# Performance work log

Measured on AMD Instinct MI355X. Metric: run time of the kernel, lower is better.

## Reference

```python
import jax, jax.numpy as jnp
import numpy as np

B, S, D, H = 2, 2048, 1024, 16
DH = D // H
DFF = 4 * D
EPS = 1e-5


def layer_norm(x, w, b):
    m = jnp.mean(x, axis=-1, keepdims=True)
    v = jnp.mean((x - m) ** 2, axis=-1, keepdims=True)
    return (x - m) / jnp.sqrt(v + EPS) * w + b


def setup_inputs() -> dict:
    key = jax.random.key(0)
    ks = jax.random.split(key, 12)
    s = 0.02
    x = jax.random.normal(ks[0], (B, S, D), dtype=jnp.float32)
    mask = jnp.tril(jnp.ones((S, S), dtype=jnp.int32))  # causal mask, 0 = blocked
    Wq = jax.random.normal(ks[1], (H, D, DH), dtype=jnp.float32) * s
    Wk = jax.random.normal(ks[2], (H, D, DH), dtype=jnp.float32) * s
    Wv = jax.random.normal(ks[3], (H, D, DH), dtype=jnp.float32) * s
    Wo = jax.random.normal(ks[4], (D, D), dtype=jnp.float32) * s
    bo = jnp.zeros((D,), dtype=jnp.float32)
    W1 = jax.random.normal(ks[5], (D, DFF), dtype=jnp.float32) * s
    b1 = jnp.zeros((DFF,), dtype=jnp.float32)
    W2 = jax.random.normal(ks[6], (DFF, D), dtype=jnp.float32) * s
    b2 = jnp.zeros((D,), dtype=jnp.float32)
    ln1_w = jnp.ones((D,), dtype=jnp.float32)
    ln1_b = jnp.zeros((D,), dtype=jnp.float32)
    ln2_w = jnp.ones((D,), dtype=jnp.float32)
    ln2_b = jnp.zeros((D,), dtype=jnp.float32)
    return {"x": x, "mask": mask, "Wq": Wq, "Wk": Wk, "Wv": Wv, "Wo": Wo,
            "bo": bo, "W1": W1, "b1": b1, "W2": W2, "b2": b2,
            "ln1_w": ln1_w, "ln1_b": ln1_b, "ln2_w": ln2_w, "ln2_b": ln2_b}


def reference(x, mask, Wq, Wk, Wv, Wo, bo, W1, b1, W2, b2,
              ln1_w, ln1_b, ln2_w, ln2_b):
    # --- pre-LN attention ---
    xn = layer_norm(x, ln1_w, ln1_b)
    q = jnp.einsum('bsd,hdk->bhsk', xn, Wq)  # [B,H,S,DH]
    k = jnp.einsum('bsd,hdk->bhsk', xn, Wk)
    v = jnp.einsum('bsd,hdk->bhsk', xn, Wv)
    scores = jnp.einsum('bhik,bhjk->bhij', q, k) / jnp.sqrt(jnp.float32(DH))
    scores = jnp.where(mask == 0, jnp.float32(-1e9), scores)  # mask broadcasts [S,S]->[B,H,S,S]
    attn = jax.nn.softmax(scores, axis=-1)
    o = jnp.einsum('bhij,bhjk->bhik', attn, v)        # [B,H,S,DH]
    o = o.transpose(0, 2, 1, 3).reshape(x.shape[0], x.shape[1], D)  # concat heads
    attn_out = o @ Wo + bo
    x = x + attn_out
    # --- pre-LN FFN ---
    xn2 = layer_norm(x, ln2_w, ln2_b)
    h = jax.nn.relu(xn2 @ W1 + b1)
    x = x + (h @ W2 + b2)
    return x
```

## Files before the change

### kernel.cpp

```cpp
#include <hip/hip_runtime.h>
#include <hip/hip_bf16.h>
#include <stdint.h>

#define DEV static __device__ __forceinline__

using f32x4  = __attribute__((ext_vector_type(4))) float;
using bf16x8 = __attribute__((ext_vector_type(8))) __bf16;

constexpr int SEQ = 2048;

DEV unsigned short f2bf(float f) {
  union { float f; unsigned u; } c; c.f = f;
  unsigned u = c.u;
  u += 0x7fffu + ((u >> 16) & 1u);
  return (unsigned short)(u >> 16);
}

DEV float wred_sum(float v) {
  #pragma unroll
  for (int m = 32; m > 0; m >>= 1) v += __shfl_xor(v, m, 64);
  return v;
}

DEV void g2l16(const unsigned short* g, unsigned short* l) {
  __builtin_amdgcn_global_load_lds(
      (const __attribute__((address_space(1))) void*)g,
      (__attribute__((address_space(3))) void*)l, 16, 0, 0);
}

DEV int xcd_map(int bid, int nwg) {
  const int cpx = nwg >> 3;
  return (bid & 7) * cpx + (bid >> 3);
}

__global__ __launch_bounds__(256) void convw_kernel(
    const float* __restrict__ in, unsigned short* __restrict__ out,
    int K, int Nh)
{
  const int h = blockIdx.z;
  const float* inh = in + (size_t)h * K * Nh;
  unsigned short* outh = out + (size_t)h * Nh * K;
  const int n0 = blockIdx.x * 32, k0 = blockIdx.y * 32;
  __shared__ float t[32][33];
  const int tx = threadIdx.x & 31, ty = threadIdx.x >> 5;
  #pragma unroll
  for (int r = 0; r < 32; r += 8)
    t[ty + r][tx] = inh[(size_t)(k0 + ty + r) * Nh + (n0 + tx)];
  __syncthreads();
  #pragma unroll
  for (int r = 0; r < 32; r += 8)
    outh[(size_t)(n0 + ty + r) * K + (k0 + tx)] = f2bf(t[tx][ty + r]);
}

__global__ __launch_bounds__(256) void ln_kernel(
    const float* __restrict__ x, const float* __restrict__ w,
    const float* __restrict__ b, unsigned short* __restrict__ out)
{
  const int row = blockIdx.x;
  const int tid = threadIdx.x;
  const float4 v = ((const float4*)(x + (size_t)row * 1024))[tid];
  float s  = v.x + v.y + v.z + v.w;
  float s2 = v.x*v.x + v.y*v.y + v.z*v.z + v.w*v.w;
  s = wred_sum(s); s2 = wred_sum(s2);
  __shared__ float rs[4], rs2[4];
  const int wave = tid >> 6, lane = tid & 63;
  if (lane == 0) { rs[wave] = s; rs2[wave] = s2; }
  __syncthreads();
  const float S  = rs[0] + rs[1] + rs[2] + rs[3];
  const float S2 = rs2[0] + rs2[1] + rs2[2] + rs2[3];
  const float mean = S * (1.f / 1024.f);
  const float var  = S2 * (1.f / 1024.f) - mean * mean;
  const float inv  = rsqrtf(var + 1e-5f);
  const float4 wv = ((const float4*)w)[tid];
  const float4 bv = ((const float4*)b)[tid];
  ushort4 o;
  o.x = f2bf((v.x - mean) * inv * wv.x + bv.x);
  o.y = f2bf((v.y - mean) * inv * wv.y + bv.y);
  o.z = f2bf((v.z - mean) * inv * wv.z + bv.z);
  o.w = f2bf((v.w - mean) * inv * wv.w + bv.w);
  ((ushort4*)(out + (size_t)row * 1024))[tid] = o;
}

#define BM 128
#define BK 32
template<int EPI, int BNT>
__global__ __launch_bounds__(256) void gemm_bt(
    const unsigned short* __restrict__ A, const unsigned short* __restrict__ BT,
    void* __restrict__ Cout, const float* __restrict__ bias,
    const float* __restrict__ res, int M, int N, int K)
{
  constexpr int NF = BNT / 32;
  __shared__ unsigned short sA[2][BM * BK];
  __shared__ unsigned short sB[2][BNT * BK];
  const int tid = threadIdx.x;
  const int wave = tid >> 6, lane = tid & 63;
  const int wr = wave >> 1, wc = wave & 1;
  const int bid = xcd_map(blockIdx.y * gridDim.x + blockIdx.x, gridDim.x * gridDim.y);
  const int m0 = (bid / gridDim.x) * BM, n0 = (bid % gridDim.x) * BNT;
  const int lr = lane & 15, lg = lane >> 4;
  const int wb = tid & 192;

  const f32x4 zero = {0.f, 0.f, 0.f, 0.f};
  f32x4 acc[4][NF];
  #pragma unroll
  for (int i = 0; i < 4; ++i)
    #pragma unroll
    for (int j = 0; j < NF; ++j) acc[i][j] = zero;

  auto STAGE = [&](int buf, int k0) {
    #pragma unroll
    for (int r = 0; r < 2; ++r) {
      const int c = tid + 256 * r;
      const int row = c >> 2, off = (c & 3) * 8;
      g2l16(A + (size_t)(m0 + row) * K + k0 + off, sA[buf] + (size_t)(r * 256 + wb) * 8);
    }
    #pragma unroll
    for (int r = 0; r < BNT / 64; ++r) {
      const int c = tid + 256 * r;
      const int row = c >> 2, off = (c & 3) * 8;
      g2l16(BT + (size_t)(n0 + row) * K + k0 + off, sB[buf] + (size_t)(r * 256 + wb) * 8);
    }
  };

  const int nt = K / BK;
  STAGE(0, 0);
  __syncthreads();
  for (int t = 0; t < nt; ++t) {
    const int buf = t & 1;
    if (t + 1 < nt) STAGE(buf ^ 1, (t + 1) * BK);
    bf16x8 af[4], bfr[NF];
    #pragma unroll
    for (int i = 0; i < 4; ++i)
      af[i] = *(const bf16x8*)(sA[buf] + (wr * 64 + i * 16 + lr) * BK + lg * 8);
    #pragma unroll
    for (int j = 0; j < NF; ++j)
      bfr[j] = *(const bf16x8*)(sB[buf] + (wc * (BNT / 2) + j * 16 + lr) * BK + lg * 8);
    #pragma unroll
    for (int i = 0; i < 4; ++i)
      #pragma unroll
      for (int j = 0; j < NF; ++j)
        acc[i][j] = __builtin_amdgcn_mfma_f32_16x16x32_bf16(af[i], bfr[j], acc[i][j], 0, 0, 0);
    __syncthreads();
  }
  #pragma unroll
  for (int i = 0; i < 4; ++i) {
    #pragma unroll
    for (int j = 0; j < NF; ++j) {
      #pragma unroll
      for (int r = 0; r < 4; ++r) {
        const int row = m0 + wr * 64 + i * 16 + lg * 4 + r;
        const int col = n0 + wc * (BNT / 2) + j * 16 + lr;
        const float v = acc[i][j][r];
        if (EPI == 0) {
          ((unsigned short*)Cout)[(size_t)row * N + col] = f2bf(v);
        } else if (EPI == 1) {
          ((float*)Cout)[(size_t)row * N + col] = v + bias[col] + res[(size_t)row * N + col];
        } else {
          float t2 = v + bias[col];
          t2 = t2 > 0.f ? t2 : 0.f;
          ((unsigned short*)Cout)[(size_t)row * N + col] = f2bf(t2);
        }
      }
    }
  }
}

template<int EPI>
__global__ __launch_bounds__(512) void gemm256(
    const unsigned short* __restrict__ A, const unsigned short* __restrict__ BT,
    void* __restrict__ Cout, const float* __restrict__ bias,
    int M, int N, int K)
{
  __shared__ unsigned short sA[2][256 * 64];
  __shared__ unsigned short sB[2][256 * 64];
  const int tid = threadIdx.x;
  const int lane = tid & 63;
  const int wave = tid >> 6;
  const int wm = wave >> 2, wn = wave & 3;
  const int bid = xcd_map(blockIdx.y * gridDim.x + blockIdx.x, gridDim.x * gridDim.y);
  const int m0 = (bid / gridDim.x) * 256, n0 = (bid % gridDim.x) * 256;
  const int lr = lane & 15, lg = lane >> 4;

  const f32x4 zero = {0.f, 0.f, 0.f, 0.f};
  f32x4 acc[8][4];
  #pragma unroll
  for (int i = 0; i < 8; ++i)
    #pragma unroll
    for (int j = 0; j < 4; ++j) acc[i][j] = zero;

  auto STAGE = [&](int buf, int k0) {
    #pragma unroll
    for (int r = 0; r < 4; ++r) {
      const int c = tid + 512 * r;
      const int row = c >> 3;
      const int slot = (c & 7) ^ (row & 7);
      const int cb = (tid & 448) + 512 * r;
      g2l16(A  + (size_t)(m0 + row) * K + k0 + slot * 8, sA[buf] + (size_t)cb * 8);
      g2l16(BT + (size_t)(n0 + row) * K + k0 + slot * 8, sB[buf] + (size_t)cb * 8);
    }
  };
  auto RD = [&](const unsigned short* base, int R, int C) -> const bf16x8* {
    return (const bf16x8*)(base + R * 64 + ((((C >> 3) ^ (R & 7))) << 3));
  };

  const int nt = K / 64;
  STAGE(0, 0);
  asm volatile("s_waitcnt vmcnt(0)" ::: "memory");
  __syncthreads();

  for (int t = 0; t < nt; ++t) {
    const int buf = t & 1;
    if (t + 1 < nt) STAGE(buf ^ 1, (t + 1) * 64);
    #pragma unroll
    for (int p = 0; p < 4; ++p) {
      const int ih = p >> 1, jh = p & 1;
      bf16x8 af[4][2], bfr[2][2];
      #pragma unroll
      for (int i = 0; i < 4; ++i)
        #pragma unroll
        for (int kk = 0; kk < 2; ++kk)
          af[i][kk] = *RD(sA[buf], wm * 128 + (ih * 4 + i) * 16 + lr, kk * 32 + lg * 8);
      #pragma unroll
      for (int j = 0; j < 2; ++j)
        #pragma unroll
        for (int kk = 0; kk < 2; ++kk)
          bfr[j][kk] = *RD(sB[buf], wn * 64 + (jh * 2 + j) * 16 + lr, kk * 32 + lg * 8);
      __builtin_amdgcn_s_setprio(1);
      #pragma unroll
      for (int i = 0; i < 4; ++i)
        #pragma unroll
        for (int j = 0; j < 2; ++j)
          #pragma unroll
          for (int kk = 0; kk < 2; ++kk)
            acc[ih * 4 + i][jh * 2 + j] = __builtin_amdgcn_mfma_f32_16x16x32_bf16(
                af[i][kk], bfr[j][kk], acc[ih * 4 + i][jh * 2 + j], 0, 0, 0);
      __builtin_amdgcn_s_setprio(0);
      if (p < 3) __builtin_amdgcn_s_barrier();
    }
    asm volatile("s_waitcnt vmcnt(0)" ::: "memory");
    __builtin_amdgcn_s_barrier();
  }

  #pragma unroll
  for (int i = 0; i < 8; ++i) {
    #pragma unroll
    for (int j = 0; j < 4; ++j) {
      #pragma unroll
      for (int r = 0; r < 4; ++r) {
        const int row = m0 + wm * 128 + i * 16 + lg * 4 + r;
        const int col = n0 + wn * 64 + j * 16 + lr;
        const float v = acc[i][j][r];
        if (EPI == 0) {
          ((unsigned short*)Cout)[(size_t)row * N + col] = f2bf(v);
        } else {
          float t2 = v + bias[col];
          t2 = t2 > 0.f ? t2 : 0.f;
          ((unsigned short*)Cout)[(size_t)row * N + col] = f2bf(t2);
        }
      }
    }
  }
}

constexpr int PAD  = 72;
constexpr int VPAD = 136;

__global__ __launch_bounds__(256) void attn_mfma(
    const unsigned short* __restrict__ qkv, unsigned short* __restrict__ o)
{
  const int p  = blockIdx.x >> 5;
  const int bh = blockIdx.x & 31;
  const int b = bh >> 4, h = bh & 15;
  const int tid = threadIdx.x;
  const int wave = tid >> 6, lane = tid & 63;
  const int lr = lane & 15, lg = lane >> 4;
  const float SC = 0.125f * 1.44269504089f;

  __shared__ unsigned short Ks[128 * PAD];
  __shared__ unsigned short Vs[64 * VPAD];
  __shared__ unsigned short Ps[4][16 * VPAD];

  #pragma unroll 1
  for (int ph = 0; ph < 2; ++ph) {
    const int qi = ph ? (31 - p) : p;
    const int q0 = qi * 64;

    const size_t qbase = ((size_t)(b * SEQ + q0 + wave * 16 + lr)) * 3072 + h * 64;
    bf16x8 qb[2];
    qb[0] = *(const bf16x8*)(qkv + qbase + lg * 8);
    qb[1] = *(const bf16x8*)(qkv + qbase + 32 + lg * 8);

    const f32x4 zero = {0.f, 0.f, 0.f, 0.f};
    f32x4 o_acc[4];
    #pragma unroll
    for (int dn = 0; dn < 4; ++dn) o_acc[dn] = zero;
    float m_run = -1e30f, l_run = 0.f;

    const int ntiles = (qi + 2) >> 1;
    for (int t = 0; t < ntiles; ++t) {
      const int j0 = t * 128;
      __syncthreads();
      #pragma unroll
      for (int r = 0; r < 4; ++r) {
        const int c = tid + 256 * r;
        const int row = c >> 3, seg = c & 7;
        const size_t base = ((size_t)(b * SEQ + j0 + row)) * 3072 + 1024 + h * 64 + seg * 8;
        *(int4*)(Ks + row * PAD + seg * 8) = *(const int4*)(qkv + base);
      }
      #pragma unroll
      for (int r = 0; r < 4; ++r) {
        const int c = tid + 256 * r;
        const int key = c & 127, dseg = c >> 7;
        const size_t base = ((size_t)(b * SEQ + j0 + key)) * 3072 + 2048 + h * 64 + dseg * 8;
        int4 rv = *(const int4*)(qkv + base);
        const unsigned short* u = (const unsigned short*)&rv;
        #pragma unroll
        for (int e = 0; e < 8; ++e) Vs[(dseg * 8 + e) * VPAD + key] = u[e];
      }
      __syncthreads();

      f32x4 s[8];
      __builtin_amdgcn_s_setprio(1);
      #pragma unroll
      for (int n = 0; n < 8; ++n) {
        const bf16x8 kf0 = *(const bf16x8*)(Ks + (n * 16 + lr) * PAD + lg * 8);
        const bf16x8 kf1 = *(const bf16x8*)(Ks + (n * 16 + lr) * PAD + 32 + lg * 8);
        s[n] = __builtin_amdgcn_mfma_f32_16x16x32_bf16(kf0, qb[0], zero, 0, 0, 0);
        s[n] = __builtin_amdgcn_mfma_f32_16x16x32_bf16(kf1, qb[1], s[n], 0, 0, 0);
      }
      __builtin_amdgcn_s_setprio(0);

      const bool diag = (t == ntiles - 1);
      const int q = q0 + wave * 16 + lr;
      const int kbase = j0 + lg * 4;
      float zm = -3e38f;
      #pragma unroll
      for (int n = 0; n < 8; ++n)
        #pragma unroll
        for (int r = 0; r < 4; ++r) {
          float z = s[n][r] * SC;
          if (diag && (kbase + n * 16 + r > q)) z = -3e38f;
          s[n][r] = z;
          zm = fmaxf(zm, z);
        }
      zm = fmaxf(zm, __shfl_xor(zm, 16, 64));
      zm = fmaxf(zm, __shfl_xor(zm, 32, 64));
      const float mnew = fmaxf(m_run, zm);
      const float alpha = exp2f(m_run - mnew);
      m_run = mnew;
      float psum = 0.f;
      #pragma unroll
      for (int n = 0; n < 8; ++n) {
        ushort4 w;
        float p0 = exp2f(s[n][0] - mnew); psum += p0; w.x = f2bf(p0);
        float p1 = exp2f(s[n][1] - mnew); psum += p1; w.y = f2bf(p1);
        float p2 = exp2f(s[n][2] - mnew); psum += p2; w.z = f2bf(p2);
        float p3 = exp2f(s[n][3] - mnew); psum += p3; w.w = f2bf(p3);
        *(ushort4*)(&Ps[wave][lr * VPAD + n * 16 + lg * 4]) = w;
      }
      psum += __shfl_xor(psum, 16, 64);
      psum += __shfl_xor(psum, 32, 64);
      l_run = l_run * alpha + psum;

      float a4[4];
      #pragma unroll
      for (int r = 0; r < 4; ++r) a4[r] = __shfl(alpha, lg * 4 + r, 64);
      #pragma unroll
      for (int dn = 0; dn < 4; ++dn)
        #pragma unroll
        for (int r = 0; r < 4; ++r) o_acc[dn][r] *= a4[r];

      bf16x8 pa[4];
      #pragma unroll
      for (int kk = 0; kk < 4; ++kk)
        pa[kk] = *(const bf16x8*)(&Ps[wave][lr * VPAD + kk * 32 + lg * 8]);
      __builtin_amdgcn_s_setprio(1);
      #pragma unroll
      for (int dn = 0; dn < 4; ++dn) {
        #pragma unroll
        for (int kk = 0; kk < 4; ++kk) {
          const bf16x8 vf = *(const bf16x8*)(Vs + (dn * 16 + lr) * VPAD + kk * 32 + lg * 8);
          o_acc[dn] = __builtin_amdgcn_mfma_f32_16x16x32_bf16(pa[kk], vf, o_acc[dn], 0, 0, 0);
        }
      }
      __builtin_amdgcn_s_setprio(0);
    }

    float linv[4];
    #pragma unroll
    for (int r = 0; r < 4; ++r) linv[r] = 1.f / __shfl(l_run, lg * 4 + r, 64);
    #pragma unroll
    for (int r = 0; r < 4; ++r) {
      const int qq = q0 + wave * 16 + lg * 4 + r;
      const size_t obase = ((size_t)(b * SEQ + qq)) * 1024 + h * 64;
      #pragma unroll
      for (int dn = 0; dn < 4; ++dn)
        o[obase + dn * 16 + lr] = f2bf(o_acc[dn][r] * linv[r]);
    }
  }
}

extern "C" void kernel_launch(void* const* d_in, const int* in_sizes, int n_in,
                              void* d_out, int out_size, void* d_ws, size_t ws_size,
                              hipStream_t stream) {
  const float* x    = (const float*)d_in[0];
  const float* Wq   = (const float*)d_in[2];
  const float* Wk   = (const float*)d_in[3];
  const float* Wv   = (const float*)d_in[4];
  const float* Wo   = (const float*)d_in[5];
  const float* bo   = (const float*)d_in[6];
  const float* W1   = (const float*)d_in[7];
  const float* b1   = (const float*)d_in[8];
  const float* W2   = (const float*)d_in[9];
  const float* b2   = (const float*)d_in[10];
  const float* ln1w = (const float*)d_in[11];
  const float* ln1b = (const float*)d_in[12];
  const float* ln2w = (const float*)d_in[13];
  const float* ln2b = (const float*)d_in[14];

  char* ws = (char*)d_ws;
  unsigned short* WqkvT = (unsigned short*)(ws);
  unsigned short* WoT   = (unsigned short*)(ws + 6291456);
  unsigned short* W1T   = (unsigned short*)(ws + 8388608);
  unsigned short* W2T   = (unsigned short*)(ws + 16777216);
  unsigned short* xn    = (unsigned short*)(ws + 25165824);
  float*          x1    = (float*)        (ws + 33554432);
  unsigned short* qkv   = (unsigned short*)(ws + 50331648);
  unsigned short* oc    = (unsigned short*)(ws + 75497472);
  unsigned short* hbuf  = qkv;

  convw_kernel<<<dim3(2, 32, 16),  256, 0, stream>>>(Wq, WqkvT,               1024, 64);
  convw_kernel<<<dim3(2, 32, 16),  256, 0, stream>>>(Wk, WqkvT + 1024 * 1024, 1024, 64);
  convw_kernel<<<dim3(2, 32, 16),  256, 0, stream>>>(Wv, WqkvT + 2048 * 1024, 1024, 64);
  convw_kernel<<<dim3(32, 32, 1),  256, 0, stream>>>(Wo, WoT, 1024, 1024);
  convw_kernel<<<dim3(128, 32, 1), 256, 0, stream>>>(W1, W1T, 1024, 4096);
  convw_kernel<<<dim3(32, 128, 1), 256, 0, stream>>>(W2, W2T, 4096, 1024);

  ln_kernel<<<4096, 256, 0, stream>>>(x, ln1w, ln1b, xn);
  gemm256<0><<<dim3(12, 16), 512, 0, stream>>>(xn, WqkvT, qkv, nullptr, 4096, 3072, 1024);
  attn_mfma<<<512, 256, 0, stream>>>(qkv, oc);
  gemm_bt<1, 64><<<dim3(16, 32), 256, 0, stream>>>(oc, WoT, x1, bo, x, 4096, 1024, 1024);
  ln_kernel<<<4096, 256, 0, stream>>>(x1, ln2w, ln2b, xn);
  gemm256<2><<<dim3(16, 16), 512, 0, stream>>>(xn, W1T, hbuf, b1, 4096, 4096, 1024);
  gemm_bt<1, 64><<<dim3(16, 32), 256, 0, stream>>>(hbuf, W2T, (float*)d_out, b2, x1, 4096, 1024, 4096);
}
```

Before: 265.3 us.

## Use 4-stage async LDS pipeline with XOR swizzle in residual GEMMs

Replaces the double-buffered gemm_bt with gemm_kp, which keeps a 4-slot LDS ring and three K-tiles in flight. Each step waits with an explicit vmcnt wait plus barrier instead of a full __syncthreads. LDS rows are XOR-swizzled to avoid bank conflicts on fragment reads. The aim is to hide global-load latency and LDS conflicts in the Wo and W2 GEMMs. In exchange it uses more LDS and relies on hand-tuned vmcnt counts, and the tail stages redundantly reload the last tile.

New measurement: 245.3 us. 1.08x faster.

```diff
diff --git a/kernel.cpp b/kernel.cpp
--- a/kernel.cpp
+++ b/kernel.cpp
@@ -81,84 +81,84 @@
   ((ushort4*)(out + (size_t)row * 1024))[tid] = o;
 }
 
-#define BM 128
-#define BK 32
-template<int EPI, int BNT>
-__global__ __launch_bounds__(256) void gemm_bt(
+template<int EPI>
+__global__ __launch_bounds__(256) void gemm_kp(
     const unsigned short* __restrict__ A, const unsigned short* __restrict__ BT,
     void* __restrict__ Cout, const float* __restrict__ bias,
     const float* __restrict__ res, int M, int N, int K)
 {
-  constexpr int NF = BNT / 32;
-  __shared__ unsigned short sA[2][BM * BK];
-  __shared__ unsigned short sB[2][BNT * BK];
+  __shared__ unsigned short sA[4][128 * 32];
+  __shared__ unsigned short sB[4][64 * 32];
   const int tid = threadIdx.x;
   const int wave = tid >> 6, lane = tid & 63;
   const int wr = wave >> 1, wc = wave & 1;
   const int bid = xcd_map(blockIdx.y * gridDim.x + blockIdx.x, gridDim.x * gridDim.y);
-  const int m0 = (bid / gridDim.x) * BM, n0 = (bid % gridDim.x) * BNT;
+  const int m0 = (bid / gridDim.x) * 128, n0 = (bid % gridDim.x) * 64;
   const int lr = lane & 15, lg = lane >> 4;
   const int wb = tid & 192;
 
   const f32x4 zero = {0.f, 0.f, 0.f, 0.f};
-  f32x4 acc[4][NF];
+  f32x4 acc[4][2];
   #pragma unroll
   for (int i = 0; i < 4; ++i)
     #pragma unroll
-    for (int j = 0; j < NF; ++j) acc[i][j] = zero;
-
-  auto STAGE = [&](int buf, int k0) {
+    for (int j = 0; j < 2; ++j) acc[i][j] = zero;
+
+  auto STAGE = [&](int slot, int kt) {
+    const int k0 = kt * 32;
     #pragma unroll
     for (int r = 0; r < 2; ++r) {
       const int c = tid + 256 * r;
-      const int row = c >> 2, off = (c & 3) * 8;
-      g2l16(A + (size_t)(m0 + row) * K + k0 + off, sA[buf] + (size_t)(r * 256 + wb) * 8);
-    }
-    #pragma unroll
-    for (int r = 0; r < BNT / 64; ++r) {
-      const int c = tid + 256 * r;
-      const int row = c >> 2, off = (c & 3) * 8;
-      g2l16(BT + (size_t)(n0 + row) * K + k0 + off, sB[buf] + (size_t)(r * 256 + wb) * 8);
-    }
+      const int row = c >> 2;
+      const int so = ((c & 3) ^ ((row >> 1) & 3)) * 8;
+      g2l16(A + (size_t)(m0 + row) * K + k0 + so, sA[slot] + (size_t)(r * 256 + wb) * 8);
+    }
+    const int row = tid >> 2;
+    const int so = ((tid & 3) ^ ((row >> 1) & 3)) * 8;
+    g2l16(BT + (size_t)(n0 + row) * K + k0 + so, sB[slot] + (size_t)wb * 8);
   };
 
-  const int nt = K / BK;
-  STAGE(0, 0);
-  __syncthreads();
+  const int nt = K / 32;
+  STAGE(0, 0); STAGE(1, 1); STAGE(2, 2);
+
   for (int t = 0; t < nt; ++t) {
-    const int buf = t & 1;
-    if (t + 1 < nt) STAGE(buf ^ 1, (t + 1) * BK);
-    bf16x8 af[4], bfr[NF];
+    asm volatile("s_waitcnt vmcnt(6)" ::: "memory");
+    __builtin_amdgcn_s_barrier();
+    const int slot = t & 3;
+    bf16x8 af[4], bfr[2];
+    #pragma unroll
+    for (int i = 0; i < 4; ++i) {
+      const int row = wr * 64 + i * 16 + lr;
+      af[i] = *(const bf16x8*)(sA[slot] + row * 32 + ((lg ^ ((row >> 1) & 3)) << 3));
+    }
+    #pragma unroll
+    for (int j = 0; j < 2; ++j) {
+      const int row = wc * 32 + j * 16 + lr;
+      bfr[j] = *(const bf16x8*)(sB[slot] + row * 32 + ((lg ^ ((row >> 1) & 3)) << 3));
+    }
     #pragma unroll
     for (int i = 0; i < 4; ++i)
-      af[i] = *(const bf16x8*)(sA[buf] + (wr * 64 + i * 16 + lr) * BK + lg * 8);
-    #pragma unroll
-    for (int j = 0; j < NF; ++j)
-      bfr[j] = *(const bf16x8*)(sB[buf] + (wc * (BNT / 2) + j * 16 + lr) * BK + lg * 8);
-    #pragma unroll
-    for (int i = 0; i < 4; ++i)
-      #pragma unroll
-      for (int j = 0; j < NF; ++j)
+      #pragma unroll
+      for (int j = 0; j < 2; ++j)
         acc[i][j] = __builtin_amdgcn_mfma_f32_16x16x32_bf16(af[i], bfr[j], acc[i][j], 0, 0, 0);
-    __syncthreads();
+    const int nx = (t + 3 < nt) ? t + 3 : nt - 1;
+    STAGE((t + 3) & 3, nx);
   }
+  asm volatile("s_waitcnt vmcnt(0)" ::: "memory");
+
   #pragma unroll
   for (int i = 0; i < 4; ++i) {
     #pragma unroll
-    for (int j = 0; j < NF; ++j) {
+    for (int j = 0; j < 2; ++j) {
       #pragma unroll
       for (int r = 0; r < 4; ++r) {
         const int row = m0 + wr * 64 + i * 16 + lg * 4 + r;
-        const int col = n0 + wc * (BNT / 2) + j * 16 + lr;
+        const int col = n0 + wc * 32 + j * 16 + lr;
         const float v = acc[i][j][r];
-        if (EPI == 0) {
-          ((unsigned short*)Cout)[(size_t)row * N + col] = f2bf(v);
-        } else if (EPI == 1) {
+        if (EPI == 1) {
           ((float*)Cout)[(size_t)row * N + col] = v + bias[col] + res[(size_t)row * N + col];
         } else {
-          float t2 = v + bias[col];
-          t2 = t2 > 0.f ? t2 : 0.f;
-          ((unsigned short*)Cout)[(size_t)row * N + col] = f2bf(t2);
+          ((unsigned short*)Cout)[(size_t)row * N + col] = f2bf(v);
         }
       }
     }
@@ -439,8 +439,8 @@
   ln_kernel<<<4096, 256, 0, stream>>>(x, ln1w, ln1b, xn);
   gemm256<0><<<dim3(12, 16), 512, 0, stream>>>(xn, WqkvT, qkv, nullptr, 4096, 3072, 1024);
   attn_mfma<<<512, 256, 0, stream>>>(qkv, oc);
-  gemm_bt<1, 64><<<dim3(16, 32), 256, 0, stream>>>(oc, WoT, x1, bo, x, 4096, 1024, 1024);
+  gemm_kp<1><<<dim3(16, 32), 256, 0, stream>>>(oc, WoT, x1, bo, x, 4096, 1024, 1024);
   ln_kernel<<<4096, 256, 0, stream>>>(x1, ln2w, ln2b, xn);
   gemm256<2><<<dim3(16, 16), 512, 0, stream>>>(xn, W1T, hbuf, b1, 4096, 4096, 1024);
-  gemm_bt<1, 64><<<dim3(16, 32), 256, 0, stream>>>(hbuf, W2T, (float*)d_out, b2, x1, 4096, 1024, 4096);
-}
+  gemm_kp<1><<<dim3(16, 32), 256, 0, stream>>>(hbuf, W2T, (float*)d_out, b2, x1, 4096, 1024, 4096);
+}
```
